# Performance work log

Measured on AMD Instinct MI355X. Metric: run time of the kernel, lower is better.

## Reference

```python
import jax, jax.numpy as jnp
import numpy as np

B, S = 32, 1024
D_MODEL, N_LABEL, D_H, D_HH, N_HEAD, N_LAYER = 1024, 8192, 64, 64, 16, 4
EPS = 1e-12

def _sq(x):
    return jnp.sum(x * x, axis=-1, keepdims=True)

def expmap0(v):
    # exponential map at the origin of the Poincare ball (c=1)
    n = jnp.sqrt(jnp.clip(_sq(v), EPS))
    return jnp.tanh(n) * v / n

def p2k(p):
    # Poincare -> Klein
    return 2.0 * p / (1.0 + _sq(p))

def k2p(k):
    # Klein -> Poincare
    return k / (1.0 + jnp.sqrt(jnp.clip(1.0 - _sq(k), EPS)))

def hyperboloid(x, klein=False):
    # lift Poincare (default) or Klein point to the hyperboloid (Lorentz) model
    sq = _sq(x)
    if klein:
        d = jnp.sqrt(jnp.clip(1.0 - sq, EPS))
        return jnp.concatenate([jnp.ones_like(sq), x], -1) / d
    return jnp.concatenate([1.0 + sq, 2.0 * x], -1) / jnp.clip(1.0 - sq, EPS)

def dist_h(u, v):
    # pairwise Lorentzian distance: u [..., n, D+1], v [..., m, D+1] -> [..., n, m]
    inner = jnp.matmul(u, jnp.swapaxes(v, -1, -2)) \
        - 2.0 * u[..., 0][..., :, None] * v[..., 0][..., None, :]
    return jnp.arccosh(jnp.clip(-inner, 1.0 + 1e-6))

def setup_inputs():
    key = jax.random.key(0)
    ks = jax.random.split(key, 12)
    def lin(k, i, o):
        return jax.random.normal(k, (i, o), jnp.float32) / float(np.sqrt(i))
    return {
        "e": jax.random.normal(ks[0], (B, S, D_MODEL), jnp.float32),
        # label embeddings kept strictly inside the unit ball (pretrained-style)
        "label": (jax.random.uniform(ks[1], (N_LABEL, D_H), jnp.float32) * 2.0 - 1.0) * float(0.5 / np.sqrt(D_H)),
        "tc_w1": lin(ks[2], D_MODEL, 2 * D_MODEL), "tc_b1": jnp.zeros((2 * D_MODEL,), jnp.float32),
        "tc_w2": lin(ks[3], 2 * D_MODEL, D_HH * N_HEAD), "tc_b2": jnp.zeros((D_HH * N_HEAD,), jnp.float32),
        "hyp_w": lin(ks[4], D_HH, D_H), "hyp_b": jnp.zeros((D_H,), jnp.float32),
        "agg_w1": lin(ks[5], N_HEAD, 2 * N_HEAD), "agg_b1": jnp.zeros((2 * N_HEAD,), jnp.float32),
        "agg_w2": lin(ks[6], 2 * N_HEAD, 2 * N_HEAD), "agg_b2": jnp.zeros((2 * N_HEAD,), jnp.float32),
        "agg_w3": lin(ks[7], 2 * N_HEAD, N_HEAD), "agg_b3": jnp.zeros((N_HEAD,), jnp.float32),
        "agg_w4": lin(ks[8], N_HEAD, 1), "agg_b4": jnp.zeros((1,), jnp.float32),
        "y": jax.random.randint(ks[9], (B, 1), 0, N_LABEL, jnp.int32),
        "mask_text": jax.random.randint(ks[10], (B, S), 0, 2, jnp.int32),
        "mask_label": jax.random.randint(ks[11], (B, N_LABEL), 0, 2, jnp.int32),
    }

def reference(e, label, tc_w1, tc_b1, tc_w2, tc_b2, hyp_w, hyp_b,
              agg_w1, agg_b1, agg_w2, agg_b2, agg_w3, agg_b3, agg_w4, agg_b4,
              y, mask_text, mask_label):
    # textconv + torch-style .view(B, n_head, S, d_hh) (pure reshape)
    h = jax.nn.relu(e @ tc_w1 + tc_b1) @ tc_w2 + tc_b2            # [B,S,H*d_hh]
    h = h.reshape(B, N_HEAD, S, D_HH)
    ek = expmap0(h @ hyp_w + hyp_b)                                # [B,H,S,d_h] Poincare ball
    q = jnp.broadcast_to(label[y][:, None], (B, N_HEAD, 1, D_H))   # [B,H,1,d_h]
    mask = mask_text[:, None, None, :] > 0                         # [B,1,1,S]
    kh = hyperboloid(ek)                                           # [B,H,S,d_h+1]
    vk = p2k(ek)                                                   # Klein coords for midpoint
    gamma = 1.0 / jnp.sqrt(jnp.clip(1.0 - _sq(vk), EPS))           # Lorentz factors [B,H,S,1]
    g = gamma[..., 0][:, :, None, :]                               # [B,H,1,S]
    # HyperbolicPathSearch: n_layer steps of distance-softmax + Einstein midpoint
    for _ in range(N_LAYER):
        scores = -dist_h(hyperboloid(q), kh)                       # [B,H,1,S]
        w = jax.nn.softmax(jnp.where(mask, scores, -1e9), axis=-1)
        wg = w * g
        mid = jnp.einsum('bhqs,bhsd->bhqd', wg, vk) / jnp.sum(wg, -1, keepdims=True)
        q = k2p(mid)
    # distance from attention output to every label embedding
    d = dist_h(hyperboloid(q), hyperboloid(label)[None, None])     # [B,H,1,n_label]
    d = jnp.squeeze(d, 2).transpose(0, 2, 1)                       # [B,n_label,H]
    x = jax.nn.relu(d @ agg_w1 + agg_b1)
    x = jax.nn.relu(x @ agg_w2 + agg_b2)
    x = jax.nn.relu(x @ agg_w3 + agg_b3)
    out = (x @ agg_w4 + agg_b4)[..., 0]                            # [B,n_label]
    return jnp.where(mask_label > 0, out, -500.0)
```

## Files before the change

kernel.cpp:

```cpp
#include <hip/hip_runtime.h>
#include <stdint.h>


typedef unsigned short u16;
typedef unsigned char u8;
typedef __attribute__((ext_vector_type(4))) float f32x4;
typedef __attribute__((ext_vector_type(4))) int i32x4;
typedef __attribute__((ext_vector_type(8))) int i32x8;

#define DEVI static __device__ __forceinline__

DEVI float bf2f(u16 u) { return __uint_as_float(((unsigned int)u) << 16); }
DEVI u16 f2bfbits(float f) {
  unsigned int x = __float_as_uint(f);
  unsigned int r = x + 0x7fffu + ((x >> 16) & 1u);
  return (u16)(r >> 16);
}
DEVI u8 f2fp8(float f) {
  return (u8)(__builtin_amdgcn_cvt_pk_fp8_f32(f, 0.f, 0, false) & 0xff);
}
DEVI unsigned int pack4_fp8(float a, float b, float c, float d) {
  int r = __builtin_amdgcn_cvt_pk_fp8_f32(a, b, 0, false);
  r = __builtin_amdgcn_cvt_pk_fp8_f32(c, d, r, true);
  return (unsigned int)r;
}

typedef __attribute__((address_space(1))) unsigned int gu32;
typedef __attribute__((address_space(3))) unsigned int su32;
DEVI void lds_cp16(const void* g, void* l) {
  __builtin_amdgcn_global_load_lds((gu32*)g, (su32*)l, 16, 0, 0);
}

__global__ __launch_bounds__(256) void prep_kernel(
    const float* __restrict__ e, const float* __restrict__ w1,
    const float* __restrict__ w2, const float* __restrict__ b2,
    const float* __restrict__ hw, const float* __restrict__ hb,
    const float* __restrict__ label,
    u8* __restrict__ e8, u8* __restrict__ w1T8, u8* __restrict__ w2eT8,
    float* __restrict__ beff, u16* __restrict__ lh0, u16* __restrict__ lhg) {
  __shared__ float t[64][65];
  const int blk = blockIdx.x;
  const int tid = threadIdx.x;

  if (blk >= 673) {
    int gi = (blk - 673) * 256 + tid;
    const float4* in = (const float4*)e + (size_t)gi * 4;
    float4 f0 = in[0], f1 = in[1], f2 = in[2], f3 = in[3];
    uint4 o;
    o.x = pack4_fp8(f0.x, f0.y, f0.z, f0.w);
    o.y = pack4_fp8(f1.x, f1.y, f1.z, f1.w);
    o.z = pack4_fp8(f2.x, f2.y, f2.z, f2.w);
    o.w = pack4_fp8(f3.x, f3.y, f3.z, f3.w);
    ((uint4*)e8)[gi] = o;
  } else if (blk < 512) {
    int c0 = (blk & 31) * 64, r0 = (blk >> 5) * 64;
    int tx = tid & 63, ty = tid >> 6;
#pragma unroll
    for (int i = 0; i < 16; i++) {
      int r = i * 4 + ty;
      t[r][tx] = w1[(size_t)(r0 + r) * 2048 + c0 + tx];
    }
    __syncthreads();
#pragma unroll
    for (int i = 0; i < 16; i++) {
      int c = i * 4 + ty;
      w1T8[(size_t)(c0 + c) * 1024 + r0 + tx] = f2fp8(t[tx][c] * 32.f);
    }
  } else if (blk < 640) {
    int bw = blk - 512;
    int ch = bw >> 3, kb = bw & 7;
    int k = kb * 256 + tid;
    float row[64];
    const float4* rp = (const float4*)(w2 + (size_t)k * 1024 + ch * 64);
#pragma unroll
    for (int i = 0; i < 16; i++) {
      float4 f = rp[i];
      row[i * 4] = f.x; row[i * 4 + 1] = f.y; row[i * 4 + 2] = f.z; row[i * 4 + 3] = f.w;
    }
    for (int o = 0; o < 64; o++) {
      float a = 0.f;
#pragma unroll
      for (int d = 0; d < 64; d++) a = fmaf(row[d], hw[d * 64 + o], a);
      w2eT8[(size_t)(ch * 64 + o) * 2048 + k] = f2fp8(a * 64.f);
    }
  } else if (blk == 640) {
    for (int n = tid; n < 1024; n += 256) {
      int ch = n >> 6, o = n & 63;
      float a = hb[o];
#pragma unroll
      for (int d = 0; d < 64; d++) a += b2[ch * 64 + d] * hw[d * 64 + o];
      beff[n] = a;
    }
  } else {
    int l = (blk - 641) * 256 + tid;
    const float4* lp = (const float4*)(label + (size_t)l * 64);
    float v[64]; float sq = 0.f;
#pragma unroll
    for (int i = 0; i < 16; i++) {
      float4 f = lp[i];
      v[i * 4] = f.x; v[i * 4 + 1] = f.y; v[i * 4 + 2] = f.z; v[i * 4 + 3] = f.w;
      sq += f.x * f.x + f.y * f.y + f.z * f.z + f.w * f.w;
    }
    float dd = fmaxf(1.f - sq, 1e-12f);
    lh0[l] = f2bfbits((1.f + sq) / dd);
    float sc = 2.f / dd;
#pragma unroll
    for (int g = 0; g < 8; g++) {
      unsigned int o0 = f2bfbits(v[8 * g + 0] * sc) | ((unsigned int)f2bfbits(v[8 * g + 1] * sc) << 16);
      unsigned int o1 = f2bfbits(v[8 * g + 2] * sc) | ((unsigned int)f2bfbits(v[8 * g + 3] * sc) << 16);
      unsigned int o2 = f2bfbits(v[8 * g + 4] * sc) | ((unsigned int)f2bfbits(v[8 * g + 5] * sc) << 16);
      unsigned int o3 = f2bfbits(v[8 * g + 6] * sc) | ((unsigned int)f2bfbits(v[8 * g + 7] * sc) << 16);
      ((uint4*)lhg)[(size_t)g * 8192 + l] = make_uint4(o0, o1, o2, o3);
    }
  }
}

template <int MODE>
__global__ __launch_bounds__(256, 4) void gemm_mx(
    const u8* __restrict__ A, const u8* __restrict__ Bt,
    const float* __restrict__ bias, u8* __restrict__ C,
    u16* __restrict__ khg, u16* __restrict__ kh0,
    int N, int K, unsigned int sb_scale) {
  __shared__ __attribute__((aligned(16))) u8 SM[32768];
  u8* As = SM;
  u8* Bs = SM + 16384;
  const int tid = threadIdx.x;
  const int wave = tid >> 6, lane = tid & 63;
  const int fr = lane & 15, q = lane >> 4;
  const int nblk = N >> 7;
  const int g = blockIdx.x;
  const int xcd = g & 7;
  const int t = g >> 3;
  const int per = (gridDim.x >> 3) / nblk;
  const int bm = xcd * per + t / nblk;
  const int bn = t % nblk;
  const size_t m0 = (size_t)bm * 128;
  const int n0 = bn * 128;
  const int wm = (wave >> 1) << 6, wn = (wave & 1) << 6;
  f32x4 acc[4][4] = {};

  const int srow = tid >> 3;
  const int schunk = (tid & 7) ^ (srow & 7);
  const u8* Ap = A + (m0 + srow) * (size_t)K + schunk * 16;
  const u8* Bp = Bt + ((size_t)n0 + srow) * K + schunk * 16;

  const int aL = (wm + fr) * 128 + ((((q << 1)) ^ (fr & 7)) << 4);
  const int bL = (wn + fr) * 128 + ((((q << 1)) ^ (fr & 7)) << 4);

  for (int kk = 0; kk < K; kk += 128) {
#pragma unroll
    for (int c = 0; c < 4; c++) {
      lds_cp16(Ap + (size_t)c * 32 * K, As + c * 4096 + wave * 1024);
      lds_cp16(Bp + (size_t)c * 32 * K, Bs + c * 4096 + wave * 1024);
    }
    Ap += 128; Bp += 128;
    __syncthreads();
    i32x8 af[4], bf[4];
#pragma unroll
    for (int t2 = 0; t2 < 4; t2++) {
      i32x4 lo = *(const i32x4*)(As + aL + t2 * 2048);
      i32x4 hi = *(const i32x4*)(As + (aL ^ 16) + t2 * 2048);
      af[t2] = __builtin_shufflevector(lo, hi, 0, 1, 2, 3, 4, 5, 6, 7);
      i32x4 lo2 = *(const i32x4*)(Bs + bL + t2 * 2048);
      i32x4 hi2 = *(const i32x4*)(Bs + (bL ^ 16) + t2 * 2048);
      bf[t2] = __builtin_shufflevector(lo2, hi2, 0, 1, 2, 3, 4, 5, 6, 7);
    }
#pragma unroll
    for (int i = 0; i < 4; i++)
#pragma unroll
      for (int j = 0; j < 4; j++)
        acc[i][j] = __builtin_amdgcn_mfma_scale_f32_16x16x128_f8f6f4(
            af[i], bf[j], acc[i][j], 0, 0,
            0, 0x7F7F7F7F,
            0, (int)sb_scale);
    __syncthreads();
  }

  if constexpr (MODE == 0) {
#pragma unroll
    for (int j = 0; j < 4; j++) {
      int col = n0 + wn + j * 16 + fr;
      float bv = bias[col];
#pragma unroll
      for (int i = 0; i < 4; i++) {
#pragma unroll
        for (int r = 0; r < 4; r++) {
          size_t row = m0 + wm + i * 16 + q * 4 + r;
          C[row * N + col] = f2fp8(fmaxf(acc[i][j][r] + bv, 0.f));
        }
      }
    }
  } else {
    u16* ew = (u16*)SM;
    u16* k0w = (u16*)(SM + 9216);
    const int head = (n0 + wn) >> 6;
    const int rb = (int)m0 + wm;
    const int b = rb >> 10, s0 = rb & 1023;
    u16* gbase = khg + (size_t)(b * 16 + head) * 65536;
    float bv[4];
#pragma unroll
    for (int j = 0; j < 4; j++) bv[j] = bias[n0 + wn + j * 16 + fr];

    float ff[4][4];
#pragma unroll
    for (int i = 0; i < 4; i++) {
#pragma unroll
      for (int r = 0; r < 4; r++) {
        float v0 = acc[i][0][r] + bv[0];
        float v1 = acc[i][1][r] + bv[1];
        float v2 = acc[i][2][r] + bv[2];
        float v3 = acc[i][3][r] + bv[3];
        float ss = v0 * v0 + v1 * v1 + v2 * v2 + v3 * v3;
        ss += __shfl_xor(ss, 1); ss += __shfl_xor(ss, 2);
        ss += __shfl_xor(ss, 4); ss += __shfl_xor(ss, 8);
        float n = sqrtf(fmaxf(ss, 1e-12f));
        float ex = __expf(-2.f * n);
        float th = (1.f - ex) / (1.f + ex);
        float sq = th * th;
        float dd = fmaxf(1.f - sq, 1e-12f);
        ff[i][r] = 2.f * (th / n) / dd;
        if (fr == 0) k0w[wave * 64 + i * 16 + q * 4 + r] = f2bfbits((1.f + sq) / dd);
      }
    }
#pragma unroll
    for (int j = 0; j < 4; j++) {
#pragma unroll
      for (int i = 0; i < 4; i++)
#pragma unroll
        for (int r = 0; r < 4; r++) {
          int trow = i * 16 + q * 4 + r;
          ew[wave * 1056 + fr * 66 + trow] =
              f2bfbits((acc[i][j][r] + bv[j]) * ff[i][r]);
        }
      __syncthreads();
#pragma unroll
      for (int it = 0; it < 2; it++) {
        const u16* eb = ew + wave * 1056 + it * 8 * 66 + lane;
        unsigned int o0 = eb[0]   | ((unsigned int)eb[66]  << 16);
        unsigned int o1 = eb[132] | ((unsigned int)eb[198] << 16);
        unsigned int o2 = eb[264] | ((unsigned int)eb[330] << 16);
        unsigned int o3 = eb[396] | ((unsigned int)eb[462] << 16);
        *(uint4*)(gbase + ((size_t)(j * 2 + it) * 1024 + s0 + lane) * 8) =
            make_uint4(o0, o1, o2, o3);
      }
      __syncthreads();
    }
    if (lane < 32) {
      unsigned int dat = *(const unsigned int*)(k0w + wave * 64 + lane * 2);
      *(unsigned int*)(kh0 + (size_t)(b * 16 + head) * 1024 + s0 + lane * 2) = dat;
    }
  }
}

__global__ __launch_bounds__(256, 2) void attn_kernel(
    const u16* __restrict__ khg, const u16* __restrict__ kh0,
    const float* __restrict__ label,
    const int* __restrict__ y, const int* __restrict__ mask_text,
    float* __restrict__ qh_out) {
  const int g = blockIdx.x;
  const int b = (g & 7) * 4 + ((g >> 3) & 3);
  const int h = g >> 5;
  const int bh = b * 16 + h;
  const int tid = threadIdx.x, lane = tid & 63, wave = tid >> 6;
  __shared__ float qh[65], rtmp[4], redp[4][65];
  const u16* khb = khg + (size_t)bh * 65536;
  const u16* k0b = kh0 + (size_t)bh * 1024;

  float kh0r[4];
  unsigned int khp[4][32];
  int mt[4];
#pragma unroll
  for (int r = 0; r < 4; r++) {
    int s = r * 256 + tid;
    mt[r] = mask_text[b * 1024 + s];
    kh0r[r] = bf2f(k0b[s]);
#pragma unroll
    for (int gg = 0; gg < 8; gg++) {
      uint4 v = *(const uint4*)(khb + ((size_t)gg * 1024 + s) * 8);
      khp[r][gg * 4 + 0] = v.x;
      khp[r][gg * 4 + 1] = v.y;
      khp[r][gg * 4 + 2] = v.z;
      khp[r][gg * 4 + 3] = v.w;
    }
  }

  if (wave == 0) {
    float qv = label[(size_t)y[b] * 64 + lane];
    float sq = qv * qv;
#pragma unroll
    for (int d = 1; d < 64; d <<= 1) sq += __shfl_xor(sq, d);
    float dd = fmaxf(1.f - sq, 1e-12f);
    qh[lane + 1] = 2.f * qv / dd;
    if (lane == 0) qh[0] = (1.f + sq) / dd;
  }
  __syncthreads();

  for (int layer = 0; layer < 4; layer++) {
    float q0 = qh[0];
    float inn[4];
#pragma unroll
    for (int r = 0; r < 4; r++) inn[r] = -q0 * kh0r[r];
#pragma unroll
    for (int k = 0; k < 32; k++) {
      float qa = qh[1 + 2 * k], qb = qh[2 + 2 * k];
#pragma unroll
      for (int r = 0; r < 4; r++) {
        unsigned int p = khp[r][k];
        inn[r] = fmaf(qa, __uint_as_float(p << 16),
                 fmaf(qb, __uint_as_float(p & 0xffff0000u), inn[r]));
      }
    }
    float w[4]; float lmax = -3e38f;
#pragma unroll
    for (int r = 0; r < 4; r++) {
      float x = fmaxf(-inn[r], 1.f + 1e-6f);
      float sco = -acoshf(x);
      sco = (mt[r] > 0) ? sco : -1e9f;
      w[r] = sco;
      lmax = fmaxf(lmax, sco);
    }
#pragma unroll
    for (int d = 1; d < 64; d <<= 1) lmax = fmaxf(lmax, __shfl_xor(lmax, d));
    if (lane == 0) rtmp[wave] = lmax;
    __syncthreads();
    float m = fmaxf(fmaxf(rtmp[0], rtmp[1]), fmaxf(rtmp[2], rtmp[3]));
#pragma unroll
    for (int r = 0; r < 4; r++) w[r] = __expf(w[r] - m);

    float p0 = w[0] * kh0r[0] + w[1] * kh0r[1] + w[2] * kh0r[2] + w[3] * kh0r[3];
#pragma unroll
    for (int d = 1; d < 64; d <<= 1) p0 += __shfl_xor(p0, d);
    if (lane == 0) redp[wave][0] = p0;
#pragma unroll
    for (int k = 0; k < 32; k++) {
      float pa = 0.f, pb = 0.f;
#pragma unroll
      for (int r = 0; r < 4; r++) {
        unsigned int p = khp[r][k];
        pa = fmaf(w[r], __uint_as_float(p << 16), pa);
        pb = fmaf(w[r], __uint_as_float(p & 0xffff0000u), pb);
      }
#pragma unroll
      for (int d = 1; d < 64; d <<= 1) pa += __shfl_xor(pa, d);
#pragma unroll
      for (int d = 1; d < 64; d <<= 1) pb += __shfl_xor(pb, d);
      if (lane == 0) { redp[wave][1 + 2 * k] = pa; redp[wave][2 + 2 * k] = pb; }
    }
    __syncthreads();

    if (wave == 0) {
      float denom = redp[0][0] + redp[1][0] + redp[2][0] + redp[3][0];
      float num = redp[0][lane + 1] + redp[1][lane + 1] + redp[2][lane + 1] + redp[3][lane + 1];
      float mid = num / denom;
      float kl = mid * mid;
#pragma unroll
      for (int d = 1; d < 64; d <<= 1) kl += __shfl_xor(kl, d);
      float u = sqrtf(fmaxf(1.f - kl, 1e-12f));
      float pc = mid / (1.f + u);
      float sp = kl / ((1.f + u) * (1.f + u));
      float dd = fmaxf(1.f - sp, 1e-12f);
      qh[lane + 1] = 2.f * pc / dd;
      if (lane == 0) qh[0] = (1.f + sp) / dd;
    }
    __syncthreads();
  }
  if (tid < 65) qh_out[(size_t)bh * 65 + tid] = qh[tid];
}

__global__ __launch_bounds__(256) void label_mlp(
    const float* __restrict__ qh, const u16* __restrict__ lh0,
    const u16* __restrict__ lhg,
    const float* __restrict__ w1, const float* __restrict__ b1,
    const float* __restrict__ w2, const float* __restrict__ b2,
    const float* __restrict__ w3, const float* __restrict__ b3,
    const float* __restrict__ w4, const float* __restrict__ b4,
    const int* __restrict__ mask_label, float* __restrict__ out) {
  int blk = blockIdx.x;
  int b = blk >> 5, lb = blk & 31;
  int l = lb * 256 + threadIdx.x;
  const float* qb = qh + (size_t)b * 1040;

  float inner[16];
  float l0 = bf2f(lh0[l]);
#pragma unroll
  for (int h = 0; h < 16; h++) inner[h] = -qb[h * 65] * l0;
#pragma unroll
  for (int g = 0; g < 8; g++) {
    uint4 v = *(const uint4*)(lhg + ((size_t)g * 8192 + l) * 8);
    unsigned int pw[4] = {v.x, v.y, v.z, v.w};
#pragma unroll
    for (int p = 0; p < 4; p++) {
      int k = g * 4 + p;
      float la = __uint_as_float(pw[p] << 16);
      float lb2 = __uint_as_float(pw[p] & 0xffff0000u);
#pragma unroll
      for (int h = 0; h < 16; h++)
        inner[h] = fmaf(qb[h * 65 + 1 + 2 * k], la,
                   fmaf(qb[h * 65 + 2 + 2 * k], lb2, inner[h]));
    }
  }
  float d[16];
#pragma unroll
  for (int h = 0; h < 16; h++) d[h] = acoshf(fmaxf(-inner[h], 1.f + 1e-6f));

  float x1[32];
#pragma unroll
  for (int o = 0; o < 32; o++) {
    float a = b1[o];
#pragma unroll
    for (int h = 0; h < 16; h++) a = fmaf(d[h], w1[h * 32 + o], a);
    x1[o] = fmaxf(a, 0.f);
  }
  float x2[32];
#pragma unroll
  for (int o = 0; o < 32; o++) {
    float a = b2[o];
#pragma unroll
    for (int i = 0; i < 32; i++) a = fmaf(x1[i], w2[i * 32 + o], a);
    x2[o] = fmaxf(a, 0.f);
  }
  float x3[16];
#pragma unroll
  for (int o = 0; o < 16; o++) {
    float a = b3[o];
#pragma unroll
    for (int i = 0; i < 32; i++) a = fmaf(x2[i], w3[i * 16 + o], a);
    x3[o] = fmaxf(a, 0.f);
  }
  float acc = b4[0];
#pragma unroll
  for (int h = 0; h < 16; h++) acc = fmaf(x3[h], w4[h], acc);
  out[(size_t)b * 8192 + l] = (mask_label[(size_t)b * 8192 + l] > 0) ? acc : -500.0f;
}

extern "C" void kernel_launch(void* const* d_in, const int* in_sizes, int n_in,
                              void* d_out, int out_size, void* d_ws, size_t ws_size,
                              hipStream_t stream) {
  const float* e     = (const float*)d_in[0];
  const float* label = (const float*)d_in[1];
  const float* tc_w1 = (const float*)d_in[2];
  const float* tc_b1 = (const float*)d_in[3];
  const float* tc_w2 = (const float*)d_in[4];
  const float* tc_b2 = (const float*)d_in[5];
  const float* hyp_w = (const float*)d_in[6];
  const float* hyp_b = (const float*)d_in[7];
  const float* aw1 = (const float*)d_in[8];
  const float* ab1 = (const float*)d_in[9];
  const float* aw2 = (const float*)d_in[10];
  const float* ab2 = (const float*)d_in[11];
  const float* aw3 = (const float*)d_in[12];
  const float* ab3 = (const float*)d_in[13];
  const float* aw4 = (const float*)d_in[14];
  const float* ab4 = (const float*)d_in[15];
  const int* y          = (const int*)d_in[16];
  const int* mask_text  = (const int*)d_in[17];
  const int* mask_label = (const int*)d_in[18];
  float* out = (float*)d_out;

  char* ws = (char*)d_ws;
  u8*    X8    = (u8*)(ws + 0);
  float* qh    = (float*)(ws + 0);
  u16*   khg   = (u16*)(ws + 67108864ull);
  u16*   kh0   = (u16*)(ws + 134217728ull);
  u8*    e8    = (u8*)(ws + 135266304ull);
  u8*    w1T8  = (u8*)(ws + 168820736ull);
  u8*    w2eT8 = (u8*)(ws + 170917888ull);
  float* beff  = (float*)(ws + 173015040ull);
  u16*   lhg   = (u16*)(ws + 173019136ull);
  u16*   lh0   = (u16*)(ws + 174067712ull);

  prep_kernel<<<673 + 8192, 256, 0, stream>>>(e, tc_w1, tc_w2, tc_b2, hyp_w, hyp_b,
                                              label, e8, w1T8, w2eT8, beff, lh0, lhg);
  gemm_mx<0><<<4096, 256, 0, stream>>>(e8, w1T8, tc_b1, X8, nullptr, nullptr,
                                       2048, 1024, 0x7A7A7A7Au);
  gemm_mx<1><<<2048, 256, 0, stream>>>(X8, w2eT8, beff, nullptr, khg, kh0,
                                       1024, 2048, 0x79797979u);
  attn_kernel<<<512, 256, 0, stream>>>(khg, kh0, label, y, mask_text, qh);
  label_mlp<<<1024, 256, 0, stream>>>(qh, lh0, lhg, aw1, ab1, aw2, ab2, aw3, ab3,
                                      aw4, ab4, mask_label, out);
}
```

Measured before the change: 553.3 us.

## Enlarge MX-FP8 GEMM tiles to 256x256 with double-buffered LDS pipeline

Rewrites the FP8 scaled-MFMA GEMM to use 512-thread blocks computing 256x256 tiles, with a two-stage LDS double buffer (128 KB) that prefetches the next K-slice while MFMAs run. Fragment loads and MFMA clusters are interleaved with explicit barriers, waitcnt and setprio to overlap LDS reads with matrix math. The larger tile raises data reuse per global byte and cuts block count. The cost is lower occupancy, with 128 KB LDS allowing at most one block per CU, and a more fragile hand-scheduled pipeline. The epilogues are adapted to the 8x4 accumulator layout.

```diff
diff --git a/kernel.cpp b/kernel.cpp
--- a/kernel.cpp
+++ b/kernel.cpp
@@ -116,94 +116,157 @@
 }
 
 template <int MODE>
-__global__ __launch_bounds__(256, 4) void gemm_mx(
+__global__ __launch_bounds__(512, 2) void gemm_mx(
     const u8* __restrict__ A, const u8* __restrict__ Bt,
     const float* __restrict__ bias, u8* __restrict__ C,
     u16* __restrict__ khg, u16* __restrict__ kh0,
     int N, int K, unsigned int sb_scale) {
-  __shared__ __attribute__((aligned(16))) u8 SM[32768];
-  u8* As = SM;
-  u8* Bs = SM + 16384;
+  __shared__ __attribute__((aligned(16))) u8 SM[131072];
   const int tid = threadIdx.x;
   const int wave = tid >> 6, lane = tid & 63;
   const int fr = lane & 15, q = lane >> 4;
-  const int nblk = N >> 7;
+  const int nblk = N >> 8;
   const int g = blockIdx.x;
   const int xcd = g & 7;
-  const int t = g >> 3;
+  const int tt = g >> 3;
   const int per = (gridDim.x >> 3) / nblk;
-  const int bm = xcd * per + t / nblk;
-  const int bn = t % nblk;
-  const size_t m0 = (size_t)bm * 128;
-  const int n0 = bn * 128;
-  const int wm = (wave >> 1) << 6, wn = (wave & 1) << 6;
-  f32x4 acc[4][4] = {};
-
-  const int srow = tid >> 3;
-  const int schunk = (tid & 7) ^ (srow & 7);
-  const u8* Ap = A + (m0 + srow) * (size_t)K + schunk * 16;
-  const u8* Bp = Bt + ((size_t)n0 + srow) * K + schunk * 16;
-
-  const int aL = (wm + fr) * 128 + ((((q << 1)) ^ (fr & 7)) << 4);
-  const int bL = (wn + fr) * 128 + ((((q << 1)) ^ (fr & 7)) << 4);
-
-  for (int kk = 0; kk < K; kk += 128) {
-#pragma unroll
-    for (int c = 0; c < 4; c++) {
-      lds_cp16(Ap + (size_t)c * 32 * K, As + c * 4096 + wave * 1024);
-      lds_cp16(Bp + (size_t)c * 32 * K, Bs + c * 4096 + wave * 1024);
-    }
-    Ap += 128; Bp += 128;
-    __syncthreads();
-    i32x8 af[4], bf[4];
-#pragma unroll
-    for (int t2 = 0; t2 < 4; t2++) {
-      i32x4 lo = *(const i32x4*)(As + aL + t2 * 2048);
-      i32x4 hi = *(const i32x4*)(As + (aL ^ 16) + t2 * 2048);
-      af[t2] = __builtin_shufflevector(lo, hi, 0, 1, 2, 3, 4, 5, 6, 7);
-      i32x4 lo2 = *(const i32x4*)(Bs + bL + t2 * 2048);
-      i32x4 hi2 = *(const i32x4*)(Bs + (bL ^ 16) + t2 * 2048);
-      bf[t2] = __builtin_shufflevector(lo2, hi2, 0, 1, 2, 3, 4, 5, 6, 7);
-    }
-#pragma unroll
-    for (int i = 0; i < 4; i++)
-#pragma unroll
-      for (int j = 0; j < 4; j++)
-        acc[i][j] = __builtin_amdgcn_mfma_scale_f32_16x16x128_f8f6f4(
-            af[i], bf[j], acc[i][j], 0, 0,
-            0, 0x7F7F7F7F,
-            0, (int)sb_scale);
-    __syncthreads();
+  const int bm = xcd * per + tt / nblk;
+  const int bn = tt % nblk;
+  const size_t m0 = (size_t)bm * 256;
+  const int n0 = bn * 256;
+  const int wm = (wave >> 2) << 7;
+  const int wn = (wave & 3) << 6;
+  f32x4 acc[8][4] = {};
+
+  const int srow8 = tid >> 3;
+  const int schunk = (tid & 7) ^ (srow8 & 7);
+  const u8* Ap = A + (m0 + srow8) * (size_t)K + schunk * 16;
+  const u8* Bp = Bt + ((size_t)n0 + srow8) * K + schunk * 16;
+  const int ldsw = wave * 1024;
+
+  const int swz = (((q << 1)) ^ (fr & 7)) << 4;
+  const int aoff = (wm + fr) * 128 + swz;
+  const int boff = (wn + fr) * 128 + swz;
+
+#define STAGE(q_, kk_)                                                     \
+  {                                                                        \
+    u8* as_ = SM + (q_) * 65536;                                           \
+    u8* bs_ = SM + (q_) * 65536 + 32768;                                   \
+    const u8* ag_ = Ap + (kk_);                                            \
+    const u8* bg_ = Bp + (kk_);                                            \
+    lds_cp16(ag_, as_ + ldsw);                                             \
+    lds_cp16(bg_, bs_ + ldsw);                                             \
+    lds_cp16(ag_ + (size_t)64 * K, as_ + 8192 + ldsw);                     \
+    lds_cp16(bg_ + (size_t)64 * K, bs_ + 8192 + ldsw);                     \
+    lds_cp16(ag_ + (size_t)128 * K, as_ + 16384 + ldsw);                   \
+    lds_cp16(bg_ + (size_t)128 * K, bs_ + 16384 + ldsw);                   \
+    lds_cp16(ag_ + (size_t)192 * K, as_ + 24576 + ldsw);                   \
+    lds_cp16(bg_ + (size_t)192 * K, bs_ + 24576 + ldsw);                   \
+  }
+
+#define LDFRAG(dst, base, off)                                             \
+  {                                                                        \
+    i32x4 lo_ = *(const i32x4*)((base) + (off));                           \
+    i32x4 hi_ = *(const i32x4*)((base) + ((off) ^ 16));                    \
+    dst = __builtin_shufflevector(lo_, hi_, 0, 1, 2, 3, 4, 5, 6, 7);       \
+  }
+
+#define MFMA_CLUSTER(mb, nb)                                               \
+  __builtin_amdgcn_s_setprio(1);                                           \
+  _Pragma("unroll") for (int mi = 0; mi < 4; mi++)                         \
+      _Pragma("unroll") for (int ni = 0; ni < 2; ni++)                     \
+          acc[(mb) + mi][(nb) + ni] =                                      \
+      __builtin_amdgcn_mfma_scale_f32_16x16x128_f8f6f4(                    \
+          af[mi], bf[(nb) + ni], acc[(mb) + mi][(nb) + ni], 0, 0,          \
+          0, 0x7F7F7F7F, 0, (int)sb_scale);                                \
+  __builtin_amdgcn_s_setprio(0);
+
+#define BAR() __builtin_amdgcn_s_barrier()
+#define SFENCE() __builtin_amdgcn_sched_barrier(0)
+#define LGKM0()                                               \
+  asm volatile("s_waitcnt lgkmcnt(0)" ::: "memory");          \
+  SFENCE()
+
+  const int NT = K >> 7;
+  STAGE(0, 0);
+  STAGE(1, 128);
+  i32x8 af[4], bf[4];
+
+  for (int t2 = 0; t2 < NT; t2++) {
+    const int cur = t2 & 1;
+    const u8* as_ = SM + cur * 65536;
+    const u8* bs_ = SM + cur * 65536 + 32768;
+    if (t2 + 1 < NT) {
+      asm volatile("s_waitcnt vmcnt(8)" ::: "memory");
+    } else {
+      asm volatile("s_waitcnt vmcnt(0)" ::: "memory");
+    }
+    SFENCE();
+    BAR();
+    SFENCE();
+    LDFRAG(af[0], as_, aoff);
+    LDFRAG(af[1], as_, aoff + 2048);
+    LDFRAG(af[2], as_, aoff + 4096);
+    LDFRAG(af[3], as_, aoff + 6144);
+    LDFRAG(bf[0], bs_, boff);
+    LDFRAG(bf[1], bs_, boff + 2048);
+    BAR();
+    LGKM0();
+    MFMA_CLUSTER(0, 0);
+    SFENCE();
+    BAR();
+    SFENCE();
+    LDFRAG(bf[2], bs_, boff + 4096);
+    LDFRAG(bf[3], bs_, boff + 6144);
+    BAR();
+    LGKM0();
+    MFMA_CLUSTER(0, 2);
+    SFENCE();
+    BAR();
+    SFENCE();
+    LDFRAG(af[0], as_, aoff + 8192);
+    LDFRAG(af[1], as_, aoff + 10240);
+    LDFRAG(af[2], as_, aoff + 12288);
+    LDFRAG(af[3], as_, aoff + 14336);
+    BAR();
+    LGKM0();
+    MFMA_CLUSTER(4, 2);
+    SFENCE();
+    BAR();
+    SFENCE();
+    if (t2 + 2 < NT) STAGE(cur, (size_t)(t2 + 2) * 128);
+    MFMA_CLUSTER(4, 0);
+    SFENCE();
   }
 
   if constexpr (MODE == 0) {
 #pragma unroll
-    for (int j = 0; j < 4; j++) {
-      int col = n0 + wn + j * 16 + fr;
+    for (int n = 0; n < 4; n++) {
+      int col = n0 + wn + n * 16 + fr;
       float bv = bias[col];
 #pragma unroll
-      for (int i = 0; i < 4; i++) {
+      for (int i = 0; i < 8; i++) {
 #pragma unroll
         for (int r = 0; r < 4; r++) {
           size_t row = m0 + wm + i * 16 + q * 4 + r;
-          C[row * N + col] = f2fp8(fmaxf(acc[i][j][r] + bv, 0.f));
+          C[row * N + col] = f2fp8(fmaxf(acc[i][n][r] + bv, 0.f));
         }
       }
     }
   } else {
     u16* ew = (u16*)SM;
-    u16* k0w = (u16*)(SM + 9216);
+    u16* k0w = (u16*)(SM + 33280);
     const int head = (n0 + wn) >> 6;
     const int rb = (int)m0 + wm;
     const int b = rb >> 10, s0 = rb & 1023;
     u16* gbase = khg + (size_t)(b * 16 + head) * 65536;
     float bv[4];
 #pragma unroll
-    for (int j = 0; j < 4; j++) bv[j] = bias[n0 + wn + j * 16 + fr];
-
-    float ff[4][4];
-#pragma unroll
-    for (int i = 0; i < 4; i++) {
+    for (int n = 0; n < 4; n++) bv[n] = bias[n0 + wn + n * 16 + fr];
+
+    float ff[8][4];
+#pragma unroll
+    for (int i = 0; i < 8; i++) {
 #pragma unroll
       for (int r = 0; r < 4; r++) {
         float v0 = acc[i][0][r] + bv[0];
@@ -219,37 +282,47 @@
         float sq = th * th;
         float dd = fmaxf(1.f - sq, 1e-12f);
         ff[i][r] = 2.f * (th / n) / dd;
-        if (fr == 0) k0w[wave * 64 + i * 16 + q * 4 + r] = f2bfbits((1.f + sq) / dd);
+        if (fr == 0) k0w[wave * 128 + i * 16 + q * 4 + r] = f2bfbits((1.f + sq) / dd);
       }
     }
 #pragma unroll
-    for (int j = 0; j < 4; j++) {
-#pragma unroll
-      for (int i = 0; i < 4; i++)
+    for (int n = 0; n < 4; n++) {
+#pragma unroll
+      for (int i = 0; i < 8; i++)
 #pragma unroll
         for (int r = 0; r < 4; r++) {
           int trow = i * 16 + q * 4 + r;
-          ew[wave * 1056 + fr * 66 + trow] =
-              f2bfbits((acc[i][j][r] + bv[j]) * ff[i][r]);
+          ew[wave * 2080 + fr * 130 + trow] =
+              f2bfbits((acc[i][n][r] + bv[n]) * ff[i][r]);
         }
       __syncthreads();
 #pragma unroll
       for (int it = 0; it < 2; it++) {
-        const u16* eb = ew + wave * 1056 + it * 8 * 66 + lane;
-        unsigned int o0 = eb[0]   | ((unsigned int)eb[66]  << 16);
-        unsigned int o1 = eb[132] | ((unsigned int)eb[198] << 16);
-        unsigned int o2 = eb[264] | ((unsigned int)eb[330] << 16);
-        unsigned int o3 = eb[396] | ((unsigned int)eb[462] << 16);
-        *(uint4*)(gbase + ((size_t)(j * 2 + it) * 1024 + s0 + lane) * 8) =
-            make_uint4(o0, o1, o2, o3);
+#pragma unroll
+        for (int it2 = 0; it2 < 2; it2++) {
+          const u16* eb = ew + wave * 2080 + it * 8 * 130 + it2 * 64 + lane;
+          unsigned int o0 = eb[0]   | ((unsigned int)eb[130] << 16);
+          unsigned int o1 = eb[260] | ((unsigned int)eb[390] << 16);
+          unsigned int o2 = eb[520] | ((unsigned int)eb[650] << 16);
+          unsigned int o3 = eb[780] | ((unsigned int)eb[910] << 16);
+          *(uint4*)(gbase +
+                    ((size_t)(n * 2 + it) * 1024 + s0 + it2 * 64 + lane) * 8) =
+              make_uint4(o0, o1, o2, o3);
+        }
       }
       __syncthreads();
     }
-    if (lane < 32) {
-      unsigned int dat = *(const unsigned int*)(k0w + wave * 64 + lane * 2);
+    {
+      unsigned int dat = ((const unsigned int*)k0w)[wave * 64 + lane];
       *(unsigned int*)(kh0 + (size_t)(b * 16 + head) * 1024 + s0 + lane * 2) = dat;
     }
   }
+#undef STAGE
+#undef LDFRAG
+#undef MFMA_CLUSTER
+#undef BAR
+#undef SFENCE
+#undef LGKM0
 }
 
 __global__ __launch_bounds__(256, 2) void attn_kernel(
@@ -471,10 +544,10 @@
 
   prep_kernel<<<673 + 8192, 256, 0, stream>>>(e, tc_w1, tc_w2, tc_b2, hyp_w, hyp_b,
                                               label, e8, w1T8, w2eT8, beff, lh0, lhg);
-  gemm_mx<0><<<4096, 256, 0, stream>>>(e8, w1T8, tc_b1, X8, nullptr, nullptr,
+  gemm_mx<0><<<1024, 512, 0, stream>>>(e8, w1T8, tc_b1, X8, nullptr, nullptr,
                                        2048, 1024, 0x7A7A7A7Au);
-  gemm_mx<1><<<2048, 256, 0, stream>>>(X8, w2eT8, beff, nullptr, khg, kh0,
-                                       1024, 2048, 0x79797979u);
+  gemm_mx<1><<<512, 512, 0, stream>>>(X8, w2eT8, beff, nullptr, khg, kh0,
+                                      1024, 2048, 0x79797979u);
   attn_kernel<<<512, 256, 0, stream>>>(khg, kh0, label, y, mask_text, qh);
   label_mlp<<<1024, 256, 0, stream>>>(qh, lh0, lhg, aw1, ab1, aw2, ab2, aw3, ab3,
                                       aw4, ab4, mask_label, out);
```

Result: slower. 571.0 us (+3.2%).
